# Kernel optimization log

Hardware: AMD Instinct MI355X
Metric: run time of the kernel (lower is better)

The kernel has to match this reference:

```python
import jax, jax.numpy as jnp
import numpy as np

P = 16; N_SIDE = 14; N_PATCH = 196
ENC_DIM = 1024; ENC_DEPTH = 2; ENC_HEADS = 16; ENC_DH = 64
DEC_DIM = 512; DEC_DEPTH = 1; DEC_HEADS = 8; DEC_DH = 64
NUM_MASKED = int(0.75 * N_PATCH)  # 147


def _ln(x, s, b):
    m = jnp.mean(x, axis=-1, keepdims=True)
    v = jnp.var(x, axis=-1, keepdims=True)
    return (x - m) * jax.lax.rsqrt(v + 1e-5) * s + b


def _mha(x, Wqkv, Wo, heads, dh):
    B, N, _ = x.shape
    q, k, v = jnp.split(x @ Wqkv, 3, axis=-1)
    rs = lambda t: t.reshape(B, N, heads, dh).transpose(0, 2, 1, 3)
    q, k, v = rs(q), rs(k), rs(v)
    scores = jnp.einsum('bhqd,bhkd->bhqk', q, k) / jnp.sqrt(jnp.float32(dh))
    att = jax.nn.softmax(scores, axis=-1)
    o = jnp.einsum('bhqk,bhkd->bhqd', att, v).transpose(0, 2, 1, 3).reshape(B, N, heads * dh)
    return o @ Wo


def _transformer(x, params, depth, heads, dh, lnfs, lnfb):
    (ln1s, ln1b, Wqkv, Wo, ln2s, ln2b, W1, b1, W2, b2) = params
    for i in range(depth):
        x = x + _mha(_ln(x, ln1s[i], ln1b[i]), Wqkv[i], Wo[i], heads, dh)
        h = jax.nn.gelu(_ln(x, ln2s[i], ln2b[i]) @ W1[i] + b1[i])
        x = x + h @ W2[i] + b2[i]
    return _ln(x, lnfs, lnfb)


def setup_inputs() -> dict:
    key = jax.random.key(0)
    ks = jax.random.split(key, 24)
    B = 64
    w = lambda k, s: (jax.random.normal(k, s, jnp.float32) * 0.02)
    E, IE = ENC_DIM, ENC_HEADS * ENC_DH
    D, ID = DEC_DIM, DEC_HEADS * DEC_DH
    d = {}
    d['images'] = jax.random.normal(ks[0], (B, 224, 224, 3), jnp.float32)
    d['rand'] = jax.random.uniform(ks[1], (B, N_PATCH), dtype=jnp.float32)
    d['patch_W'] = w(ks[2], (P * P * 3, E)); d['patch_b'] = jnp.zeros((E,), jnp.float32)
    d['pos_emb'] = w(ks[3], (N_PATCH, E))
    d['enc_ln1s'] = jnp.ones((ENC_DEPTH, E), jnp.float32); d['enc_ln1b'] = jnp.zeros((ENC_DEPTH, E), jnp.float32)
    d['enc_Wqkv'] = w(ks[4], (ENC_DEPTH, E, 3 * IE)); d['enc_Wo'] = w(ks[5], (ENC_DEPTH, IE, E))
    d['enc_ln2s'] = jnp.ones((ENC_DEPTH, E), jnp.float32); d['enc_ln2b'] = jnp.zeros((ENC_DEPTH, E), jnp.float32)
    d['enc_W1'] = w(ks[6], (ENC_DEPTH, E, 4 * E)); d['enc_b1'] = jnp.zeros((ENC_DEPTH, 4 * E), jnp.float32)
    d['enc_W2'] = w(ks[7], (ENC_DEPTH, 4 * E, E)); d['enc_b2'] = jnp.zeros((ENC_DEPTH, E), jnp.float32)
    d['enc_lnfs'] = jnp.ones((E,), jnp.float32); d['enc_lnfb'] = jnp.zeros((E,), jnp.float32)
    d['e2d_W'] = w(ks[8], (E, D)); d['e2d_b'] = jnp.zeros((D,), jnp.float32)
    d['mask_token'] = w(ks[9], (D,))
    d['dec_pos'] = w(ks[10], (N_PATCH, D))
    d['dec_ln1s'] = jnp.ones((DEC_DEPTH, D), jnp.float32); d['dec_ln1b'] = jnp.zeros((DEC_DEPTH, D), jnp.float32)
    d['dec_Wqkv'] = w(ks[11], (DEC_DEPTH, D, 3 * ID)); d['dec_Wo'] = w(ks[12], (DEC_DEPTH, ID, D))
    d['dec_ln2s'] = jnp.ones((DEC_DEPTH, D), jnp.float32); d['dec_ln2b'] = jnp.zeros((DEC_DEPTH, D), jnp.float32)
    d['dec_W1'] = w(ks[13], (DEC_DEPTH, D, 4 * D)); d['dec_b1'] = jnp.zeros((DEC_DEPTH, 4 * D), jnp.float32)
    d['dec_W2'] = w(ks[14], (DEC_DEPTH, 4 * D, D)); d['dec_b2'] = jnp.zeros((DEC_DEPTH, D), jnp.float32)
    d['dec_lnfs'] = jnp.ones((D,), jnp.float32); d['dec_lnfb'] = jnp.zeros((D,), jnp.float32)
    d['pix_W'] = w(ks[15], (D, E)); d['pix_b'] = jnp.zeros((E,), jnp.float32)  # pixel_dim == encoder_dim per source
    return d


def reference(images, rand, patch_W, patch_b, pos_emb,
              enc_ln1s, enc_ln1b, enc_Wqkv, enc_Wo, enc_ln2s, enc_ln2b,
              enc_W1, enc_b1, enc_W2, enc_b2, enc_lnfs, enc_lnfb,
              e2d_W, e2d_b, mask_token, dec_pos,
              dec_ln1s, dec_ln1b, dec_Wqkv, dec_Wo, dec_ln2s, dec_ln2b,
              dec_W1, dec_b1, dec_W2, dec_b2, dec_lnfs, dec_lnfb,
              pix_W, pix_b):
    B = images.shape[0]
    # patch embed: [B,224,224,3] -> [B,196,768] -> [B,196,1024]
    x = images.reshape(B, N_SIDE, P, N_SIDE, P, 3).transpose(0, 1, 3, 2, 4, 5).reshape(B, N_PATCH, P * P * 3)
    patches = x @ patch_W + patch_b
    tokens = patches + pos_emb
    # random masking via argsort of uniform noise
    order = jnp.argsort(rand, axis=-1)
    m_idx = order[:, :NUM_MASKED]        # [B,147]
    u_idx = order[:, NUM_MASKED:]        # [B,49]
    unmasked = jnp.take_along_axis(tokens, u_idx[:, :, None], axis=1)
    enc_params = (enc_ln1s, enc_ln1b, enc_Wqkv, enc_Wo, enc_ln2s, enc_ln2b, enc_W1, enc_b1, enc_W2, enc_b2)
    encoded = _transformer(unmasked, enc_params, ENC_DEPTH, ENC_HEADS, ENC_DH, enc_lnfs, enc_lnfb)
    dec_tok = encoded @ e2d_W + e2d_b + dec_pos[u_idx]
    mask_toks = mask_token + dec_pos[m_idx]
    bidx = jnp.arange(B)[:, None]
    all_tok = jnp.zeros((B, N_PATCH, DEC_DIM), dec_tok.dtype)
    all_tok = all_tok.at[bidx, u_idx].set(dec_tok)
    all_tok = all_tok.at[bidx, m_idx].set(mask_toks)
    dec_params = (dec_ln1s, dec_ln1b, dec_Wqkv, dec_Wo, dec_ln2s, dec_ln2b, dec_W1, dec_b1, dec_W2, dec_b2)
    decoded = _transformer(all_tok, dec_params, DEC_DEPTH, DEC_HEADS, DEC_DH, dec_lnfs, dec_lnfb)
    pred = jnp.take_along_axis(decoded, m_idx[:, :, None], axis=1) @ pix_W + pix_b
    target = jnp.take_along_axis(patches, m_idx[:, :, None], axis=1)
    return jnp.mean((pred - target) ** 2)
```

## Files before the change

### kernel.cpp

```cpp
#include <hip/hip_runtime.h>

typedef __attribute__((ext_vector_type(8))) __bf16 bf16x8;
typedef __attribute__((ext_vector_type(4))) float f32x4;

#define OFF_PATCH 0ull
#define OFF_X     25690112ull
#define OFF_LN    51380224ull
#define OFF_QKV   64225280ull
#define OFF_HID   103022592ull
#define OFF_WP    154402816ull
#define OFF_ORD   214695936ull
#define OFF_PART  214746112ull

#define WP_PATCH   0ull
#define WP_ENC_QKV 786432ull
#define WP_ENC_WO  7077888ull
#define WP_ENC_W1  9175040ull
#define WP_ENC_W2  17563648ull
#define WP_E2D     25952256ull
#define WP_DEC_QKV 26476544ull
#define WP_DEC_WO  27262976ull
#define WP_DEC_W1  27525120ull
#define WP_DEC_W2  28573696ull
#define WP_PIX     29622272ull

#define OM_BF16 0
#define OM_F32  1
#define OM_ACC  2
#define OM_GELU 3

__device__ __forceinline__ float b2f(unsigned short u) {
    return __uint_as_float(((unsigned int)u) << 16);
}
__device__ __forceinline__ unsigned short f2b(float f) {
    unsigned int x = __float_as_uint(f);
    x += 0x7fffu + ((x >> 16) & 1u);
    return (unsigned short)(x >> 16);
}
__device__ __forceinline__ float gelu_f(float x) {
    float u2 = 1.5957691216057308f * x * (1.f + 0.044715f * x * x);
    return x / (1.f + __expf(-u2));
}
__device__ __forceinline__ void gload16(const void* g, void* l) {
    __builtin_amdgcn_global_load_lds((const __attribute__((address_space(1))) void*)g,
                                     (__attribute__((address_space(3))) void*)l, 16, 0, 0);
}

struct PackArgs {
    const float* src[15];
    unsigned long long dstOff[15];
    int K[15], N[15];
    int tileStart[16];
};
__global__ __launch_bounds__(256) void pack_all(PackArgs pa, unsigned short* __restrict__ wp) {
    __shared__ float tile[32][33];
    int t = blockIdx.x;
    int d = 0;
    while (d < 14 && t >= pa.tileStart[d + 1]) ++d;
    int local = t - pa.tileStart[d];
    int K = pa.K[d], N = pa.N[d];
    int ntn = N >> 5;
    int kt = (local / ntn) << 5, nt = (local % ntn) << 5;
    const float* in = pa.src[d];
    unsigned short* out = wp + pa.dstOff[d];
    int tx = threadIdx.x & 31, ty = threadIdx.x >> 5;
#pragma unroll
    for (int i = 0; i < 32; i += 8) tile[ty + i][tx] = in[(size_t)(kt + ty + i) * N + nt + tx];
    __syncthreads();
#pragma unroll
    for (int i = 0; i < 32; i += 8)
        out[(size_t)(nt + ty + i) * K + kt + tx] = f2b(tile[tx][ty + i]);
}

__global__ __launch_bounds__(256) void patchify_kernel(const float* __restrict__ img,
                                                       unsigned short* __restrict__ Xp) {
    const long long total = 12544ll * 768;
    for (long long e = (long long)blockIdx.x * 256 + threadIdx.x; e < total;
         e += (long long)gridDim.x * 256) {
        int row = (int)(e / 768), k = (int)(e % 768);
        int b = row / 196, pi = row % 196;
        int py = pi / 14, px = pi % 14;
        int r = k / 48, rem = k % 48;
        int c = rem / 3, ch = rem % 3;
        long long src = (((long long)(b * 224 + py * 16 + r)) * 224 + (px * 16 + c)) * 3 + ch;
        Xp[e] = f2b(img[src]);
    }
}

template <int OM, bool ATOMIC, bool GATHER>
__global__ __launch_bounds__(512) void gemmV(const unsigned short* __restrict__ A,
                                             const unsigned short* __restrict__ Bt,
                                             void* __restrict__ Cv,
                                             const float* __restrict__ bias,
                                             const int* __restrict__ gord,
                                             int M, int N, int K, int Kc) {
    __shared__ __align__(16) unsigned short S[2 * 128 * 64];
    const int tid = threadIdx.x, w = tid >> 6, lane = tid & 63;
    const int wm = w >> 1, wn = w & 1;
    int nwg = gridDim.x * gridDim.y;
    int orig = blockIdx.y * gridDim.x + blockIdx.x;
    int q = nwg >> 3, r8 = nwg & 7, xcd = orig & 7, off = orig >> 3;
    int wg = (xcd < r8 ? xcd * (q + 1) : r8 * (q + 1) + (xcd - r8) * q) + off;
    const int brow = (wg / gridDim.x) * 128, bcol = (wg % gridDim.x) * 128;
    const int kBeg = blockIdx.z * Kc;
    const int fr = lane & 15, fq = lane >> 4;
    const int lr = lane >> 3;
    const int sca = ((lane & 7) ^ lr) * 8;
    const unsigned short* Agp[2];
#pragma unroll
    for (int i = 0; i < 2; ++i) {
        int r = brow + w * 16 + i * 8 + lr;
        if (r > M - 1) r = M - 1;
        if constexpr (GATHER) {
            int bb = r / 147, jj = r - bb * 147;
            r = bb * 196 + gord[bb * 196 + jj];
        }
        Agp[i] = A + (size_t)r * K + kBeg + sca;
    }
    const unsigned short* Bgp[2];
#pragma unroll
    for (int i = 0; i < 2; ++i) {
        int r = bcol + w * 16 + i * 8 + lr;
        Bgp[i] = Bt + (size_t)r * K + kBeg + sca;
    }

    f32x4 acc[2][4];
#pragma unroll
    for (int m = 0; m < 2; ++m)
#pragma unroll
        for (int n = 0; n < 4; ++n) acc[m][n] = (f32x4){0.f, 0.f, 0.f, 0.f};

    const char* lds = (const char*)S;
    const int sw = (fr & 7) << 4;
    const int a0 = (wm * 32 + fr) * 128 + ((fq * 16) ^ sw);
    const int b0 = 16384 + (wn * 64 + fr) * 128 + ((fq * 16) ^ sw);

    const int nt = Kc >> 6;
    for (int t = 0; t < nt; ++t) {
        __syncthreads();
        const int k0 = t << 6;
#pragma unroll
        for (int i = 0; i < 2; ++i)
            gload16(Agp[i] + k0, S + (w * 16 + i * 8) * 64);
#pragma unroll
        for (int i = 0; i < 2; ++i)
            gload16(Bgp[i] + k0, S + 128 * 64 + (w * 16 + i * 8) * 64);
        __syncthreads();
#pragma unroll
        for (int kk = 0; kk < 2; ++kk) {
            const int kx = kk * 64;
            bf16x8 af[2], bf[4];
#pragma unroll
            for (int m = 0; m < 2; ++m)
                af[m] = *(const bf16x8*)(lds + ((a0 ^ kx) + m * 2048));
#pragma unroll
            for (int n = 0; n < 4; ++n)
                bf[n] = *(const bf16x8*)(lds + ((b0 ^ kx) + n * 2048));
#pragma unroll
            for (int m = 0; m < 2; ++m)
#pragma unroll
                for (int n = 0; n < 4; ++n)
                    acc[m][n] = __builtin_amdgcn_mfma_f32_16x16x32_bf16(af[m], bf[n],
                                                                       acc[m][n], 0, 0, 0);
        }
    }

    const bool addBias = (bias != nullptr) && (kBeg == 0);
#pragma unroll
    for (int m = 0; m < 2; ++m) {
        int rb = brow + wm * 32 + m * 16 + fq * 4;
#pragma unroll
        for (int r = 0; r < 4; ++r) {
            int row = rb + r;
            if (row < M) {
#pragma unroll
                for (int n = 0; n < 4; ++n) {
                    int col = bcol + wn * 64 + n * 16 + fr;
                    float v = acc[m][n][r];
                    if (addBias) v += bias[col];
                    size_t o = (size_t)row * N + col;
                    if constexpr (ATOMIC) atomicAdd((float*)Cv + o, v);
                    else if constexpr (OM == OM_BF16) ((unsigned short*)Cv)[o] = f2b(v);
                    else if constexpr (OM == OM_F32) ((float*)Cv)[o] = v;
                    else if constexpr (OM == OM_ACC) ((float*)Cv)[o] += v;
                    else ((unsigned short*)Cv)[o] = f2b(gelu_f(v));
                }
            }
        }
    }
}

template <int OM>
__global__ __launch_bounds__(256) void gemm3s(const unsigned short* __restrict__ A,
                                              const unsigned short* __restrict__ Bt,
                                              void* __restrict__ Cv,
                                              const float* __restrict__ bias,
                                              int M, int N, int K) {
    __shared__ __align__(16) unsigned short S[2 * 128 * 64];
    const int tid = threadIdx.x, wave = tid >> 6, lane = tid & 63;
    int nwg = gridDim.x * gridDim.y;
    int orig = blockIdx.y * gridDim.x + blockIdx.x;
    int q = nwg >> 3, r8 = nwg & 7, xcd = orig & 7, off = orig >> 3;
    int wg = (xcd < r8 ? xcd * (q + 1) : r8 * (q + 1) + (xcd - r8) * q) + off;
    const int brow = (wg / gridDim.x) * 128, bcol = (wg % gridDim.x) * 128;
    const int fr = lane & 15, fq = lane >> 4;
    const int wr = (wave >> 1) * 64, wc = (wave & 1) * 64;
    const int lr = lane >> 3;
    const int sca = ((lane & 7) ^ lr) * 8;
    const unsigned short* Agp[4];
#pragma unroll
    for (int i = 0; i < 4; ++i) {
        int r = brow + wave * 32 + i * 8 + lr;
        if (r > M - 1) r = M - 1;
        Agp[i] = A + (size_t)r * K + sca;
    }
    const unsigned short* Bgp[4];
#pragma unroll
    for (int i = 0; i < 4; ++i) {
        int r = bcol + wave * 32 + i * 8 + lr;
        Bgp[i] = Bt + (size_t)r * K + sca;
    }
    f32x4 acc[4][4];
#pragma unroll
    for (int m = 0; m < 4; ++m)
#pragma unroll
        for (int n = 0; n < 4; ++n) acc[m][n] = (f32x4){0.f, 0.f, 0.f, 0.f};
    const char* lds = (const char*)S;
    const int sw = (fr & 7) << 4;
    const int a0 = (wr + fr) * 128 + ((fq * 16) ^ sw);
    const int b0 = 16384 + (wc + fr) * 128 + ((fq * 16) ^ sw);
    const int nt = K >> 6;
    for (int t = 0; t < nt; ++t) {
        __syncthreads();
        const int k0 = t << 6;
#pragma unroll
        for (int i = 0; i < 4; ++i) {
            gload16(Agp[i] + k0, S + (wave * 32 + i * 8) * 64);
            gload16(Bgp[i] + k0, S + 128 * 64 + (wave * 32 + i * 8) * 64);
        }
        __syncthreads();
#pragma unroll
        for (int kk = 0; kk < 2; ++kk) {
            const int kx = kk * 64;
            bf16x8 af[4], bf[4];
#pragma unroll
            for (int m = 0; m < 4; ++m) af[m] = *(const bf16x8*)(lds + ((a0 ^ kx) + m * 2048));
#pragma unroll
            for (int n = 0; n < 4; ++n) bf[n] = *(const bf16x8*)(lds + ((b0 ^ kx) + n * 2048));
#pragma unroll
            for (int m = 0; m < 4; ++m)
#pragma unroll
                for (int n = 0; n < 4; ++n)
                    acc[m][n] = __builtin_amdgcn_mfma_f32_16x16x32_bf16(af[m], bf[n],
                                                                       acc[m][n], 0, 0, 0);
        }
    }
#pragma unroll
    for (int m = 0; m < 4; ++m) {
        int rb = brow + wr + m * 16 + fq * 4;
#pragma unroll
        for (int r = 0; r < 4; ++r) {
            int row = rb + r;
            if (row < M) {
#pragma unroll
                for (int n = 0; n < 4; ++n) {
                    int col = bcol + wc + n * 16 + fr;
                    float v = acc[m][n][r];
                    if (bias) v += bias[col];
                    size_t o = (size_t)row * N + col;
                    if constexpr (OM == OM_F32) ((float*)Cv)[o] = v;
                    else ((unsigned short*)Cv)[o] = f2b(v);
                }
            }
        }
    }
}

template <int N, int H, int NW>
__global__ __launch_bounds__(NW * 64) void attn_mfma(const unsigned short* __restrict__ qkv,
                                                     unsigned short* __restrict__ out) {
    constexpr int Npad = ((N + 31) / 32) * 32;
    constexpr int NT = Npad / 16;
    constexpr int KS = Npad / 32;
    constexpr int PS = Npad + 8;
    constexpr int SQ = 3 * H * 64, SO = H * 64;
    __shared__ __align__(16) unsigned short Kl[Npad * 64];
    __shared__ __align__(16) unsigned short Vt[64 * PS];
    __shared__ __align__(16) unsigned short Pl[NW * 16 * PS];
    const int b = blockIdx.x / H, h = blockIdx.x % H;
    const unsigned short* base = qkv + (size_t)b * N * SQ;
    const int qoff = h * 64, koff = (H + h) * 64, voff = (2 * H + h) * 64;
    const int tid = threadIdx.x, wave = tid >> 6, lane = tid & 63;
    const int fr = lane & 15, fq = lane >> 4;

    for (int idx = tid; idx < Npad * 8; idx += NW * 64) {
        int row = idx >> 3, ch = idx & 7;
        uint4 v = {0u, 0u, 0u, 0u};
        if (row < N) v = *(const uint4*)(base + (size_t)row * SQ + koff + ch * 8);
        *(uint4*)((char*)Kl + row * 128 + ((ch * 16) ^ ((row & 7) << 4))) = v;
    }
    for (int idx = tid; idx < Npad * 32; idx += NW * 64) {
        int key = idx >> 5, d2 = (idx & 31) * 2;
        unsigned int v = 0;
        if (key < N) v = *(const unsigned int*)(base + (size_t)key * SQ + voff + d2);
        Vt[d2 * PS + key] = (unsigned short)(v & 0xffffu);
        Vt[(d2 + 1) * PS + key] = (unsigned short)(v >> 16);
    }
    __syncthreads();

    unsigned short* pw = Pl + wave * 16 * PS;
    for (int qt = wave; qt < NT; qt += NW) {
        const int q0 = qt * 16;
        int qr = q0 + fr;
        if (qr > N - 1) qr = N - 1;
        const unsigned short* qp = base + (size_t)qr * SQ + qoff + fq * 8;
        bf16x8 aq0 = *(const bf16x8*)qp;
        bf16x8 aq1 = *(const bf16x8*)(qp + 32);
        f32x4 sa[NT];
#pragma unroll
        for (int ct = 0; ct < NT; ++ct) sa[ct] = (f32x4){0.f, 0.f, 0.f, 0.f};
#pragma unroll
        for (int ct = 0; ct < NT; ++ct) {
            const char* kb = (const char*)Kl + (ct * 16 + fr) * 128;
            bf16x8 kf0 = *(const bf16x8*)(kb + ((fq * 16) ^ ((fr & 7) << 4)));
            bf16x8 kf1 = *(const bf16x8*)(kb + ((64 + fq * 16) ^ ((fr & 7) << 4)));
            sa[ct] = __builtin_amdgcn_mfma_f32_16x16x32_bf16(aq0, kf0, sa[ct], 0, 0, 0);
            sa[ct] = __builtin_amdgcn_mfma_f32_16x16x32_bf16(aq1, kf1, sa[ct], 0, 0, 0);
        }
        float mrow[4] = {-3e38f, -3e38f, -3e38f, -3e38f};
#pragma unroll
        for (int ct = 0; ct < NT; ++ct) {
            bool ok = (ct * 16 + fr) < N;
#pragma unroll
            for (int r = 0; r < 4; ++r) {
                float s = ok ? sa[ct][r] * 0.125f : -3e38f;
                sa[ct][r] = s;
                mrow[r] = fmaxf(mrow[r], s);
            }
        }
#pragma unroll
        for (int off = 1; off <= 8; off <<= 1)
#pragma unroll
            for (int r = 0; r < 4; ++r) mrow[r] = fmaxf(mrow[r], __shfl_xor(mrow[r], off));
        float ssum[4] = {0.f, 0.f, 0.f, 0.f};
#pragma unroll
        for (int ct = 0; ct < NT; ++ct)
#pragma unroll
            for (int r = 0; r < 4; ++r) {
                float p = __expf(sa[ct][r] - mrow[r]);
                sa[ct][r] = p;
                ssum[r] += p;
            }
#pragma unroll
        for (int off = 1; off <= 8; off <<= 1)
#pragma unroll
            for (int r = 0; r < 4; ++r) ssum[r] += __shfl_xor(ssum[r], off);
#pragma unroll
        for (int ct = 0; ct < NT; ++ct)
#pragma unroll
            for (int r = 0; r < 4; ++r)
                pw[(fq * 4 + r) * PS + ct * 16 + fr] = f2b(sa[ct][r]);
        f32x4 oa[4];
#pragma unroll
        for (int vt = 0; vt < 4; ++vt) oa[vt] = (f32x4){0.f, 0.f, 0.f, 0.f};
#pragma unroll
        for (int ks = 0; ks < KS; ++ks) {
            bf16x8 pa = *(const bf16x8*)(pw + fr * PS + ks * 32 + fq * 8);
#pragma unroll
            for (int vt = 0; vt < 4; ++vt) {
                bf16x8 vf = *(const bf16x8*)(&Vt[(vt * 16 + fr) * PS + ks * 32 + fq * 8]);
                oa[vt] = __builtin_amdgcn_mfma_f32_16x16x32_bf16(pa, vf, oa[vt], 0, 0, 0);
            }
        }
        float inv[4];
#pragma unroll
        for (int r = 0; r < 4; ++r) inv[r] = 1.f / ssum[r];
#pragma unroll
        for (int vt = 0; vt < 4; ++vt)
#pragma unroll
            for (int r = 0; r < 4; ++r) {
                int q = q0 + fq * 4 + r;
                if (q < N)
                    out[((size_t)b * N + q) * SO + h * 64 + vt * 16 + fr] =
                        f2b(oa[vt][r] * inv[r]);
            }
    }
}

__global__ __launch_bounds__(256) void argsort_kernel(const float* __restrict__ rnd,
                                                      int* __restrict__ ord) {
    __shared__ float vals[196];
    int b = blockIdx.x, t = threadIdx.x;
    if (t < 196) vals[t] = rnd[b * 196 + t];
    __syncthreads();
    if (t < 196) {
        float v = vals[t];
        int rank = 0;
        for (int j = 0; j < 196; ++j) {
            float vj = vals[j];
            rank += (vj < v) || (vj == v && j < t);
        }
        ord[b * 196 + rank] = t;
    }
}

__global__ __launch_bounds__(256) void gather_unmasked(const unsigned short* __restrict__ patches,
                                                       const float* __restrict__ pos,
                                                       const int* __restrict__ ord,
                                                       float* __restrict__ xe) {
    int row = blockIdx.x;
    int b = row / 49, i = row % 49;
    int src = ord[b * 196 + 147 + i];
    const unsigned short* pr = patches + ((size_t)(b * 196 + src) << 10);
    const float* pe = pos + ((size_t)src << 10);
    float* o = xe + ((size_t)row << 10);
    int d = threadIdx.x * 4;
    ushort4 pv = *(const ushort4*)(pr + d);
    float4 p4 = *(const float4*)(pe + d);
    float4 r;
    r.x = b2f(pv.x) + p4.x; r.y = b2f(pv.y) + p4.y;
    r.z = b2f(pv.z) + p4.z; r.w = b2f(pv.w) + p4.w;
    *(float4*)(o + d) = r;
}

template <int L>
__global__ __launch_bounds__(256) void ln_kernel(const float* __restrict__ x,
                                                 unsigned short* __restrict__ y,
                                                 const float* __restrict__ sw,
                                                 const float* __restrict__ bw) {
    __shared__ float red[8];
    const int tid = threadIdx.x;
    const float* xr = x + (size_t)blockIdx.x * L;
    float sum = 0.f, sq = 0.f;
    for (int i = tid * 4; i < L; i += 1024) {
        float4 v = *(const float4*)(xr + i);
        sum += v.x + v.y + v.z + v.w;
        sq += v.x * v.x + v.y * v.y + v.z * v.z + v.w * v.w;
    }
    for (int off = 32; off; off >>= 1) {
        sum += __shfl_xor(sum, off);
        sq += __shfl_xor(sq, off);
    }
    int wave = tid >> 6, lane = tid & 63;
    if (lane == 0) { red[wave] = sum; red[4 + wave] = sq; }
    __syncthreads();
    float ts = red[0] + red[1] + red[2] + red[3];
    float tq = red[4] + red[5] + red[6] + red[7];
    float mean = ts / L;
    float inv = rsqrtf(tq / L - mean * mean + 1e-5f);
    unsigned short* yr = y + (size_t)blockIdx.x * L;
    for (int i = tid * 4; i < L; i += 1024) {
        float4 v = *(const float4*)(xr + i);
        float4 s4 = *(const float4*)(sw + i);
        float4 b4 = *(const float4*)(bw + i);
        ushort4 o;
        o.x = f2b((v.x - mean) * inv * s4.x + b4.x);
        o.y = f2b((v.y - mean) * inv * s4.y + b4.y);
        o.z = f2b((v.z - mean) * inv * s4.z + b4.z);
        o.w = f2b((v.w - mean) * inv * s4.w + b4.w);
        *(ushort4*)(yr + i) = o;
    }
}

__global__ __launch_bounds__(256) void scatter_tokens(const float* __restrict__ dec_tok,
                                                      const float* __restrict__ dec_pos,
                                                      const float* __restrict__ mask_tok,
                                                      const int* __restrict__ ord,
                                                      float* __restrict__ all_tok) {
    int e = blockIdx.x;
    int b = e / 196, i = e % 196;
    int idx = ord[e];
    float* o = all_tok + ((size_t)(b * 196 + idx)) * 512;
    const float* dp = dec_pos + (size_t)idx * 512;
    int d = threadIdx.x * 4;
    if (d < 512) {
        float4 dv = *(const float4*)(dp + d);
        float4 sv;
        if (i < 147) sv = *(const float4*)(mask_tok + d);
        else sv = *(const float4*)(dec_tok + ((size_t)(b * 49 + (i - 147))) * 512 + d);
        float4 r = {sv.x + dv.x, sv.y + dv.y, sv.z + dv.z, sv.w + dv.w};
        *(float4*)(o + d) = r;
    }
}

__global__ __launch_bounds__(256) void loss_partial(const float* __restrict__ pred,
                                                    const unsigned short* __restrict__ patches,
                                                    const int* __restrict__ ord,
                                                    float* __restrict__ part) {
    __shared__ float red[8];
    float local = 0.f;
    const long long total = 9633792ll;
    for (long long e = (long long)blockIdx.x * 256 + threadIdx.x; e < total; e += 4096ll * 256) {
        int r = (int)(e >> 10), d = (int)(e & 1023);
        int b = r / 147, j = r % 147;
        int idx = ord[b * 196 + j];
        float t = b2f(patches[(((size_t)(b * 196 + idx)) << 10) + d]);
        float df = pred[e] - t;
        local += df * df;
    }
    for (int off = 32; off; off >>= 1) local += __shfl_xor(local, off);
    int wave = threadIdx.x >> 6, lane = threadIdx.x & 63;
    if (lane == 0) red[wave] = local;
    __syncthreads();
    if (threadIdx.x == 0) part[blockIdx.x] = red[0] + red[1] + red[2] + red[3];
}

__global__ __launch_bounds__(256) void loss_final(const float* __restrict__ part,
                                                  float* __restrict__ out) {
    __shared__ float red[8];
    float local = 0.f;
    for (int i = threadIdx.x; i < 4096; i += 256) local += part[i];
    for (int off = 32; off; off >>= 1) local += __shfl_xor(local, off);
    int wave = threadIdx.x >> 6, lane = threadIdx.x & 63;
    if (lane == 0) red[wave] = local;
    __syncthreads();
    if (threadIdx.x == 0) out[0] = (red[0] + red[1] + red[2] + red[3]) / 9633792.0f;
}

extern "C" void kernel_launch(void* const* d_in, const int* in_sizes, int n_in, void* d_out,
                              int out_size, void* d_ws, size_t ws_size, hipStream_t stream) {
    const float* images = (const float*)d_in[0];
    const float* rnd = (const float*)d_in[1];
    const float* patch_W = (const float*)d_in[2];
    const float* patch_b = (const float*)d_in[3];
    const float* pos_emb = (const float*)d_in[4];
    const float* enc_ln1s = (const float*)d_in[5];
    const float* enc_ln1b = (const float*)d_in[6];
    const float* enc_Wqkv = (const float*)d_in[7];
    const float* enc_Wo = (const float*)d_in[8];
    const float* enc_ln2s = (const float*)d_in[9];
    const float* enc_ln2b = (const float*)d_in[10];
    const float* enc_W1 = (const float*)d_in[11];
    const float* enc_b1 = (const float*)d_in[12];
    const float* enc_W2 = (const float*)d_in[13];
    const float* enc_b2 = (const float*)d_in[14];
    const float* enc_lnfs = (const float*)d_in[15];
    const float* enc_lnfb = (const float*)d_in[16];
    const float* e2d_W = (const float*)d_in[17];
    const float* e2d_b = (const float*)d_in[18];
    const float* mask_tok = (const float*)d_in[19];
    const float* dec_pos = (const float*)d_in[20];
    const float* dec_ln1s = (const float*)d_in[21];
    const float* dec_ln1b = (const float*)d_in[22];
    const float* dec_Wqkv = (const float*)d_in[23];
    const float* dec_Wo = (const float*)d_in[24];
    const float* dec_ln2s = (const float*)d_in[25];
    const float* dec_ln2b = (const float*)d_in[26];
    const float* dec_W1 = (const float*)d_in[27];
    const float* dec_b1 = (const float*)d_in[28];
    const float* dec_W2 = (const float*)d_in[29];
    const float* dec_b2 = (const float*)d_in[30];
    const float* dec_lnfs = (const float*)d_in[31];
    const float* dec_lnfb = (const float*)d_in[32];
    const float* pix_W = (const float*)d_in[33];
    const float* pix_b = (const float*)d_in[34];

    char* ws = (char*)d_ws;
    unsigned short* patches = (unsigned short*)(ws + OFF_PATCH);
    float* Rx = (float*)(ws + OFF_X);
    unsigned short* Rln = (unsigned short*)(ws + OFF_LN);
    unsigned short* RqkvB = (unsigned short*)(ws + OFF_QKV);
    float* RqkvF = (float*)(ws + OFF_QKV);
    unsigned short* Rhid = (unsigned short*)(ws + OFF_HID);
    unsigned short* wp = (unsigned short*)(ws + OFF_WP);
    int* ord = (int*)(ws + OFF_ORD);
    float* part = (float*)(ws + OFF_PART);
    float* out = (float*)d_out;

    PackArgs pa;
    int nd = 0, tiles = 0;
    auto ADDP = [&](const float* src, unsigned long long wpo, int K, int N) {
        pa.src[nd] = src; pa.dstOff[nd] = wpo; pa.K[nd] = K; pa.N[nd] = N;
        pa.tileStart[nd] = tiles;
        tiles += (K >> 5) * (N >> 5);
        ++nd;
    };
    ADDP(patch_W, WP_PATCH, 768, 1024);
    for (int l = 0; l < 2; ++l) {
        ADDP(enc_Wqkv + (size_t)l * 1024 * 3072, WP_ENC_QKV + (size_t)l * 3145728, 1024, 3072);
        ADDP(enc_Wo + (size_t)l * 1024 * 1024, WP_ENC_WO + (size_t)l * 1048576, 1024, 1024);
        ADDP(enc_W1 + (size_t)l * 1024 * 4096, WP_ENC_W1 + (size_t)l * 4194304, 1024, 4096);
        ADDP(enc_W2 + (size_t)l * 4096 * 1024, WP_ENC_W2 + (size_t)l * 4194304, 4096, 1024);
    }
    ADDP(e2d_W, WP_E2D, 1024, 512);
    ADDP(dec_Wqkv, WP_DEC_QKV, 512, 1536);
    ADDP(dec_Wo, WP_DEC_WO, 512, 512);
    ADDP(dec_W1, WP_DEC_W1, 512, 2048);
    ADDP(dec_W2, WP_DEC_W2, 2048, 512);
    ADDP(pix_W, WP_PIX, 512, 1024);
    pa.tileStart[nd] = tiles;
    pack_all<<<tiles, 256, 0, stream>>>(pa, wp);

    auto GEMM = [&](int om, const unsigned short* A, size_t wpo, void* C, const float* bias,
                    int M, int N, int K, int S, bool small, const int* gord = nullptr) {
        const unsigned short* Bt = wp + wpo;
        int Kc = K / S;
        if (!small) {
            dim3 g(N / 128, (M + 127) / 128, S);
            if (gord) gemmV<OM_F32, false, true><<<g, 512, 0, stream>>>(A, Bt, C, bias, gord, M, N, K, Kc);
            else if (S > 1) gemmV<OM_ACC, true, false><<<g, 512, 0, stream>>>(A, Bt, C, bias, nullptr, M, N, K, Kc);
            else if (om == OM_BF16) gemmV<OM_BF16, false, false><<<g, 512, 0, stream>>>(A, Bt, C, bias, nullptr, M, N, K, Kc);
            else if (om == OM_F32) gemmV<OM_F32, false, false><<<g, 512, 0, stream>>>(A, Bt, C, bias, nullptr, M, N, K, Kc);
            else if (om == OM_ACC) gemmV<OM_ACC, false, false><<<g, 512, 0, stream>>>(A, Bt, C, bias, nullptr, M, N, K, Kc);
            else gemmV<OM_GELU, false, false><<<g, 512, 0, stream>>>(A, Bt, C, bias, nullptr, M, N, K, Kc);
        } else {
            dim3 g(N / 128, (M + 127) / 128, 1);
            if (om == OM_F32) gemm3s<OM_F32><<<g, 256, 0, stream>>>(A, Bt, C, bias, M, N, K);
            else gemm3s<OM_BF16><<<g, 256, 0, stream>>>(A, Bt, C, bias, M, N, K);
        }
    };

    patchify_kernel<<<4096, 256, 0, stream>>>(images, Rhid);
    GEMM(OM_BF16, Rhid, WP_PATCH, patches, patch_b, 12544, 1024, 768, 1, false);
    argsort_kernel<<<64, 256, 0, stream>>>(rnd, ord);
    gather_unmasked<<<3136, 256, 0, stream>>>(patches, pos_emb, ord, Rx);

    for (int l = 0; l < 2; ++l) {
        ln_kernel<1024><<<3136, 256, 0, stream>>>(Rx, Rln, enc_ln1s + l * 1024,
                                                  enc_ln1b + l * 1024);
        GEMM(OM_BF16, Rln, WP_ENC_QKV + (size_t)l * 3145728, RqkvB, nullptr, 3136, 3072, 1024,
             1, false);
        attn_mfma<49, 16, 4><<<64 * 16, 256, 0, stream>>>(RqkvB, Rhid);
        GEMM(OM_ACC, Rhid, WP_ENC_WO + (size_t)l * 1048576, Rx, nullptr, 3136, 1024, 1024, 4,
             false);
        ln_kernel<1024><<<3136, 256, 0, stream>>>(Rx, Rln, enc_ln2s + l * 1024,
                                                  enc_ln2b + l * 1024);
        GEMM(OM_GELU, Rln, WP_ENC_W1 + (size_t)l * 4194304, Rhid, enc_b1 + l * 4096, 3136,
             4096, 1024, 1, false);
        GEMM(OM_ACC, Rhid, WP_ENC_W2 + (size_t)l * 4194304, Rx, enc_b2 + l * 1024, 3136, 1024,
             4096, 4, false);
    }
    ln_kernel<1024><<<3136, 256, 0, stream>>>(Rx, Rln, enc_lnfs, enc_lnfb);

    GEMM(OM_F32, Rln, WP_E2D, RqkvF, e2d_b, 3136, 512, 1024, 1, true);
    scatter_tokens<<<12544, 256, 0, stream>>>(RqkvF, dec_pos, mask_tok, ord, Rx);

    ln_kernel<512><<<12544, 256, 0, stream>>>(Rx, Rln, dec_ln1s, dec_ln1b);
    GEMM(OM_BF16, Rln, WP_DEC_QKV, RqkvB, nullptr, 12544, 1536, 512, 1, false);
    attn_mfma<196, 8, 8><<<64 * 8, 512, 0, stream>>>(RqkvB, Rhid);
    GEMM(OM_ACC, Rhid, WP_DEC_WO, Rx, nullptr, 12544, 512, 512, 2, false);
    ln_kernel<512><<<12544, 256, 0, stream>>>(Rx, Rln, dec_ln2s, dec_ln2b);
    GEMM(OM_GELU, Rln, WP_DEC_W1, Rhid, dec_b1, 12544, 2048, 512, 1, false);
    GEMM(OM_ACC, Rhid, WP_DEC_W2, Rx, dec_b2, 12544, 512, 2048, 2, false);
    ln_kernel<512><<<12544, 256, 0, stream>>>(Rx, Rln, dec_lnfs, dec_lnfb);

    GEMM(OM_F32, Rln, WP_PIX, RqkvF, pix_b, 9408, 1024, 512, 1, false, ord);
    loss_partial<<<4096, 256, 0, stream>>>(RqkvF, patches, ord, part);
    loss_final<<<1, 256, 0, stream>>>(part, out);
}
```

Baseline: 844.9 us.

## Rewrite main GEMM to use 32x32x16 MFMA with 4 waves per block

The main 128x128 tiled GEMM kernel changes from 8 waves, each issuing 16x16x32 MFMAs over a 32x64 subtile, to 4 waves that each compute a 64x64 subtile with four 32x32x16 MFMAs. Each wave now loads twice as many global rows per K-step, and the LDS read pattern and epilogue indexing are adapted to the 32x32 accumulator layout. The aim is fewer LDS fragment reads per FLOP and better MFMA throughput. In exchange there are fewer waves per block for latency hiding and more accumulator registers per thread.

```diff
diff --git a/kernel.cpp b/kernel.cpp
--- a/kernel.cpp
+++ b/kernel.cpp
@@ -2,6 +2,7 @@
 
 typedef __attribute__((ext_vector_type(8))) __bf16 bf16x8;
 typedef __attribute__((ext_vector_type(4))) float f32x4;
+typedef __attribute__((ext_vector_type(16))) float f32x16;
 
 #define OFF_PATCH 0ull
 #define OFF_X     25690112ull
@@ -88,28 +89,28 @@
 }
 
 template <int OM, bool ATOMIC, bool GATHER>
-__global__ __launch_bounds__(512) void gemmV(const unsigned short* __restrict__ A,
+__global__ __launch_bounds__(256) void gemmU(const unsigned short* __restrict__ A,
                                              const unsigned short* __restrict__ Bt,
                                              void* __restrict__ Cv,
                                              const float* __restrict__ bias,
                                              const int* __restrict__ gord,
                                              int M, int N, int K, int Kc) {
     __shared__ __align__(16) unsigned short S[2 * 128 * 64];
-    const int tid = threadIdx.x, w = tid >> 6, lane = tid & 63;
-    const int wm = w >> 1, wn = w & 1;
+    const int tid = threadIdx.x, wave = tid >> 6, lane = tid & 63;
+    const int wm = wave >> 1, wn = wave & 1;
     int nwg = gridDim.x * gridDim.y;
     int orig = blockIdx.y * gridDim.x + blockIdx.x;
     int q = nwg >> 3, r8 = nwg & 7, xcd = orig & 7, off = orig >> 3;
     int wg = (xcd < r8 ? xcd * (q + 1) : r8 * (q + 1) + (xcd - r8) * q) + off;
     const int brow = (wg / gridDim.x) * 128, bcol = (wg % gridDim.x) * 128;
     const int kBeg = blockIdx.z * Kc;
-    const int fr = lane & 15, fq = lane >> 4;
+    const int l31 = lane & 31, hi = lane >> 5;
     const int lr = lane >> 3;
     const int sca = ((lane & 7) ^ lr) * 8;
-    const unsigned short* Agp[2];
-#pragma unroll
-    for (int i = 0; i < 2; ++i) {
-        int r = brow + w * 16 + i * 8 + lr;
+    const unsigned short* Agp[4];
+#pragma unroll
+    for (int i = 0; i < 4; ++i) {
+        int r = brow + wave * 32 + i * 8 + lr;
         if (r > M - 1) r = M - 1;
         if constexpr (GATHER) {
             int bb = r / 147, jj = r - bb * 147;
@@ -117,74 +118,66 @@
         }
         Agp[i] = A + (size_t)r * K + kBeg + sca;
     }
-    const unsigned short* Bgp[2];
-#pragma unroll
-    for (int i = 0; i < 2; ++i) {
-        int r = bcol + w * 16 + i * 8 + lr;
+    const unsigned short* Bgp[4];
+#pragma unroll
+    for (int i = 0; i < 4; ++i) {
+        int r = bcol + wave * 32 + i * 8 + lr;
         Bgp[i] = Bt + (size_t)r * K + kBeg + sca;
     }
 
-    f32x4 acc[2][4];
-#pragma unroll
-    for (int m = 0; m < 2; ++m)
-#pragma unroll
-        for (int n = 0; n < 4; ++n) acc[m][n] = (f32x4){0.f, 0.f, 0.f, 0.f};
+    f32x16 accA, accB, accC, accD;
+#pragma unroll
+    for (int i = 0; i < 16; ++i) { accA[i] = 0.f; accB[i] = 0.f; accC[i] = 0.f; accD[i] = 0.f; }
 
     const char* lds = (const char*)S;
-    const int sw = (fr & 7) << 4;
-    const int a0 = (wm * 32 + fr) * 128 + ((fq * 16) ^ sw);
-    const int b0 = 16384 + (wn * 64 + fr) * 128 + ((fq * 16) ^ sw);
+    const int sw = (l31 & 7) << 4;
+    const int a0 = (wm * 64 + l31) * 128;
+    const int b0 = 16384 + (wn * 64 + l31) * 128;
 
     const int nt = Kc >> 6;
     for (int t = 0; t < nt; ++t) {
         __syncthreads();
         const int k0 = t << 6;
 #pragma unroll
-        for (int i = 0; i < 2; ++i)
-            gload16(Agp[i] + k0, S + (w * 16 + i * 8) * 64);
-#pragma unroll
-        for (int i = 0; i < 2; ++i)
-            gload16(Bgp[i] + k0, S + 128 * 64 + (w * 16 + i * 8) * 64);
+        for (int i = 0; i < 4; ++i)
+            gload16(Agp[i] + k0, S + (wave * 32 + i * 8) * 64);
+#pragma unroll
+        for (int i = 0; i < 4; ++i)
+            gload16(Bgp[i] + k0, S + 128 * 64 + (wave * 32 + i * 8) * 64);
         __syncthreads();
 #pragma unroll
-        for (int kk = 0; kk < 2; ++kk) {
-            const int kx = kk * 64;
-            bf16x8 af[2], bf[4];
-#pragma unroll
-            for (int m = 0; m < 2; ++m)
-                af[m] = *(const bf16x8*)(lds + ((a0 ^ kx) + m * 2048));
-#pragma unroll
-            for (int n = 0; n < 4; ++n)
-                bf[n] = *(const bf16x8*)(lds + ((b0 ^ kx) + n * 2048));
-#pragma unroll
-            for (int m = 0; m < 2; ++m)
-#pragma unroll
-                for (int n = 0; n < 4; ++n)
-                    acc[m][n] = __builtin_amdgcn_mfma_f32_16x16x32_bf16(af[m], bf[n],
-                                                                       acc[m][n], 0, 0, 0);
+        for (int kk = 0; kk < 4; ++kk) {
+            const int ko = (kk * 32 + hi * 16) ^ sw;
+            bf16x8 af0 = *(const bf16x8*)(lds + a0 + ko);
+            bf16x8 af1 = *(const bf16x8*)(lds + a0 + 4096 + ko);
+            bf16x8 bf0 = *(const bf16x8*)(lds + b0 + ko);
+            bf16x8 bf1 = *(const bf16x8*)(lds + b0 + 4096 + ko);
+            accA = __builtin_amdgcn_mfma_f32_32x32x16_bf16(af0, bf0, accA, 0, 0, 0);
+            accB = __builtin_amdgcn_mfma_f32_32x32x16_bf16(af0, bf1, accB, 0, 0, 0);
+            accC = __builtin_amdgcn_mfma_f32_32x32x16_bf16(af1, bf0, accC, 0, 0, 0);
+            accD = __builtin_amdgcn_mfma_f32_32x32x16_bf16(af1, bf1, accD, 0, 0, 0);
         }
     }
 
     const bool addBias = (bias != nullptr) && (kBeg == 0);
-#pragma unroll
-    for (int m = 0; m < 2; ++m) {
-        int rb = brow + wm * 32 + m * 16 + fq * 4;
-#pragma unroll
-        for (int r = 0; r < 4; ++r) {
-            int row = rb + r;
+    const f32x16* accs[4] = {&accA, &accB, &accC, &accD};
+#pragma unroll
+    for (int f = 0; f < 4; ++f) {
+        const int mi = f >> 1, ni = f & 1;
+        const f32x16& ac = *accs[f];
+#pragma unroll
+        for (int r = 0; r < 16; ++r) {
+            int row = brow + wm * 64 + mi * 32 + (r & 3) + 8 * (r >> 2) + 4 * hi;
             if (row < M) {
-#pragma unroll
-                for (int n = 0; n < 4; ++n) {
-                    int col = bcol + wn * 64 + n * 16 + fr;
-                    float v = acc[m][n][r];
-                    if (addBias) v += bias[col];
-                    size_t o = (size_t)row * N + col;
-                    if constexpr (ATOMIC) atomicAdd((float*)Cv + o, v);
-                    else if constexpr (OM == OM_BF16) ((unsigned short*)Cv)[o] = f2b(v);
-                    else if constexpr (OM == OM_F32) ((float*)Cv)[o] = v;
-                    else if constexpr (OM == OM_ACC) ((float*)Cv)[o] += v;
-                    else ((unsigned short*)Cv)[o] = f2b(gelu_f(v));
-                }
+                int col = bcol + wn * 64 + ni * 32 + l31;
+                float v = ac[r];
+                if (addBias) v += bias[col];
+                size_t o = (size_t)row * N + col;
+                if constexpr (ATOMIC) atomicAdd((float*)Cv + o, v);
+                else if constexpr (OM == OM_BF16) ((unsigned short*)Cv)[o] = f2b(v);
+                else if constexpr (OM == OM_F32) ((float*)Cv)[o] = v;
+                else if constexpr (OM == OM_ACC) ((float*)Cv)[o] += v;
+                else ((unsigned short*)Cv)[o] = f2b(gelu_f(v));
             }
         }
     }
@@ -597,12 +590,12 @@
         int Kc = K / S;
         if (!small) {
             dim3 g(N / 128, (M + 127) / 128, S);
-            if (gord) gemmV<OM_F32, false, true><<<g, 512, 0, stream>>>(A, Bt, C, bias, gord, M, N, K, Kc);
-            else if (S > 1) gemmV<OM_ACC, true, false><<<g, 512, 0, stream>>>(A, Bt, C, bias, nullptr, M, N, K, Kc);
-            else if (om == OM_BF16) gemmV<OM_BF16, false, false><<<g, 512, 0, stream>>>(A, Bt, C, bias, nullptr, M, N, K, Kc);
-            else if (om == OM_F32) gemmV<OM_F32, false, false><<<g, 512, 0, stream>>>(A, Bt, C, bias, nullptr, M, N, K, Kc);
-            else if (om == OM_ACC) gemmV<OM_ACC, false, false><<<g, 512, 0, stream>>>(A, Bt, C, bias, nullptr, M, N, K, Kc);
-            else gemmV<OM_GELU, false, false><<<g, 512, 0, stream>>>(A, Bt, C, bias, nullptr, M, N, K, Kc);
+            if (gord) gemmU<OM_F32, false, true><<<g, 256, 0, stream>>>(A, Bt, C, bias, gord, M, N, K, Kc);
+            else if (S > 1) gemmU<OM_ACC, true, false><<<g, 256, 0, stream>>>(A, Bt, C, bias, nullptr, M, N, K, Kc);
+            else if (om == OM_BF16) gemmU<OM_BF16, false, false><<<g, 256, 0, stream>>>(A, Bt, C, bias, nullptr, M, N, K, Kc);
+            else if (om == OM_F32) gemmU<OM_F32, false, false><<<g, 256, 0, stream>>>(A, Bt, C, bias, nullptr, M, N, K, Kc);
+            else if (om == OM_ACC) gemmU<OM_ACC, false, false><<<g, 256, 0, stream>>>(A, Bt, C, bias, nullptr, M, N, K, Kc);
+            else gemmU<OM_GELU, false, false><<<g, 256, 0, stream>>>(A, Bt, C, bias, nullptr, M, N, K, Kc);
         } else {
             dim3 g(N / 128, (M + 127) / 128, 1);
             if (om == OM_F32) gemm3s<OM_F32><<<g, 256, 0, stream>>>(A, Bt, C, bias, M, N, K);
```

New measurement: 972.7 us. +15.1%, slower.

## Fuse MSE loss into pixel-projection GEMM epilogue and use nontemporal stores

Applied to the files above, without the earlier changes.

The pixel-projection GEMM now computes squared error against the gathered target patches directly in its epilogue. It reduces per wave and atomically adds into a single accumulator. This removes the fp32 prediction write/read round trip (~38MB) and the separate partial-reduction kernel. Other GEMM epilogue stores become nontemporal stores, and the loss sum now depends on float atomic ordering.

```diff
diff --git a/kernel.cpp b/kernel.cpp
--- a/kernel.cpp
+++ b/kernel.cpp
@@ -28,6 +28,7 @@
 #define OM_F32  1
 #define OM_ACC  2
 #define OM_GELU 3
+#define OM_LOSS 4
 
 __device__ __forceinline__ float b2f(unsigned short u) {
     return __uint_as_float(((unsigned int)u) << 16);
@@ -93,6 +94,8 @@
                                              void* __restrict__ Cv,
                                              const float* __restrict__ bias,
                                              const int* __restrict__ gord,
+                                             const unsigned short* __restrict__ tgt,
+                                             float* __restrict__ lsum,
                                              int M, int N, int K, int Kc) {
     __shared__ __align__(16) unsigned short S[2 * 128 * 64];
     const int tid = threadIdx.x, w = tid >> 6, lane = tid & 63;
@@ -166,6 +169,7 @@
     }
 
     const bool addBias = (bias != nullptr) && (kBeg == 0);
+    float lloc = 0.f;
 #pragma unroll
     for (int m = 0; m < 2; ++m) {
         int rb = brow + wm * 32 + m * 16 + fq * 4;
@@ -173,20 +177,40 @@
         for (int r = 0; r < 4; ++r) {
             int row = rb + r;
             if (row < M) {
+                size_t prow = 0;
+                if constexpr (OM == OM_LOSS) {
+                    int bb = row / 147, jj = row - bb * 147;
+                    prow = (size_t)(bb * 196 + gord[bb * 196 + jj]);
+                }
 #pragma unroll
                 for (int n = 0; n < 4; ++n) {
                     int col = bcol + wn * 64 + n * 16 + fr;
                     float v = acc[m][n][r];
                     if (addBias) v += bias[col];
-                    size_t o = (size_t)row * N + col;
-                    if constexpr (ATOMIC) atomicAdd((float*)Cv + o, v);
-                    else if constexpr (OM == OM_BF16) ((unsigned short*)Cv)[o] = f2b(v);
-                    else if constexpr (OM == OM_F32) ((float*)Cv)[o] = v;
-                    else if constexpr (OM == OM_ACC) ((float*)Cv)[o] += v;
-                    else ((unsigned short*)Cv)[o] = f2b(gelu_f(v));
+                    if constexpr (OM == OM_LOSS) {
+                        float t = b2f(tgt[(prow << 10) + col]);
+                        float d = v - t;
+                        lloc += d * d;
+                    } else {
+                        size_t o = (size_t)row * N + col;
+                        if constexpr (ATOMIC) atomicAdd((float*)Cv + o, v);
+                        else if constexpr (OM == OM_BF16)
+                            __builtin_nontemporal_store(f2b(v), (unsigned short*)Cv + o);
+                        else if constexpr (OM == OM_F32)
+                            __builtin_nontemporal_store(v, (float*)Cv + o);
+                        else if constexpr (OM == OM_ACC) ((float*)Cv)[o] += v;
+                        else
+                            __builtin_nontemporal_store(f2b(gelu_f(v)),
+                                                        (unsigned short*)Cv + o);
+                    }
                 }
             }
         }
+    }
+    if constexpr (OM == OM_LOSS) {
+#pragma unroll
+        for (int off2 = 32; off2; off2 >>= 1) lloc += __shfl_xor(lloc, off2);
+        if (lane == 0) atomicAdd(lsum, lloc);
     }
 }
 
@@ -483,38 +507,13 @@
     }
 }
 
-__global__ __launch_bounds__(256) void loss_partial(const float* __restrict__ pred,
-                                                    const unsigned short* __restrict__ patches,
-                                                    const int* __restrict__ ord,
-                                                    float* __restrict__ part) {
-    __shared__ float red[8];
-    float local = 0.f;
-    const long long total = 9633792ll;
-    for (long long e = (long long)blockIdx.x * 256 + threadIdx.x; e < total; e += 4096ll * 256) {
-        int r = (int)(e >> 10), d = (int)(e & 1023);
-        int b = r / 147, j = r % 147;
-        int idx = ord[b * 196 + j];
-        float t = b2f(patches[(((size_t)(b * 196 + idx)) << 10) + d]);
-        float df = pred[e] - t;
-        local += df * df;
-    }
-    for (int off = 32; off; off >>= 1) local += __shfl_xor(local, off);
-    int wave = threadIdx.x >> 6, lane = threadIdx.x & 63;
-    if (lane == 0) red[wave] = local;
-    __syncthreads();
-    if (threadIdx.x == 0) part[blockIdx.x] = red[0] + red[1] + red[2] + red[3];
-}
-
-__global__ __launch_bounds__(256) void loss_final(const float* __restrict__ part,
-                                                  float* __restrict__ out) {
-    __shared__ float red[8];
-    float local = 0.f;
-    for (int i = threadIdx.x; i < 4096; i += 256) local += part[i];
-    for (int off = 32; off; off >>= 1) local += __shfl_xor(local, off);
-    int wave = threadIdx.x >> 6, lane = threadIdx.x & 63;
-    if (lane == 0) red[wave] = local;
-    __syncthreads();
-    if (threadIdx.x == 0) out[0] = (red[0] + red[1] + red[2] + red[3]) / 9633792.0f;
+__global__ __launch_bounds__(64) void zero_part(float* __restrict__ part) {
+    part[threadIdx.x] = 0.f;
+}
+
+__global__ __launch_bounds__(64) void loss_final(const float* __restrict__ part,
+                                                 float* __restrict__ out) {
+    if (threadIdx.x == 0) out[0] = part[0] / 9633792.0f;
 }
 
 extern "C" void kernel_launch(void* const* d_in, const int* in_sizes, int n_in, void* d_out,
@@ -592,17 +591,18 @@
     pack_all<<<tiles, 256, 0, stream>>>(pa, wp);
 
     auto GEMM = [&](int om, const unsigned short* A, size_t wpo, void* C, const float* bias,
-                    int M, int N, int K, int S, bool small, const int* gord = nullptr) {
+                    int M, int N, int K, int S, bool small, const int* gord = nullptr,
+                    const unsigned short* tgt = nullptr, float* lsum = nullptr) {
         const unsigned short* Bt = wp + wpo;
         int Kc = K / S;
         if (!small) {
             dim3 g(N / 128, (M + 127) / 128, S);
-            if (gord) gemmV<OM_F32, false, true><<<g, 512, 0, stream>>>(A, Bt, C, bias, gord, M, N, K, Kc);
-            else if (S > 1) gemmV<OM_ACC, true, false><<<g, 512, 0, stream>>>(A, Bt, C, bias, nullptr, M, N, K, Kc);
-            else if (om == OM_BF16) gemmV<OM_BF16, false, false><<<g, 512, 0, stream>>>(A, Bt, C, bias, nullptr, M, N, K, Kc);
-            else if (om == OM_F32) gemmV<OM_F32, false, false><<<g, 512, 0, stream>>>(A, Bt, C, bias, nullptr, M, N, K, Kc);
-            else if (om == OM_ACC) gemmV<OM_ACC, false, false><<<g, 512, 0, stream>>>(A, Bt, C, bias, nullptr, M, N, K, Kc);
-            else gemmV<OM_GELU, false, false><<<g, 512, 0, stream>>>(A, Bt, C, bias, nullptr, M, N, K, Kc);
+            if (om == OM_LOSS) gemmV<OM_LOSS, false, true><<<g, 512, 0, stream>>>(A, Bt, C, bias, gord, tgt, lsum, M, N, K, Kc);
+            else if (S > 1) gemmV<OM_ACC, true, false><<<g, 512, 0, stream>>>(A, Bt, C, bias, nullptr, nullptr, nullptr, M, N, K, Kc);
+            else if (om == OM_BF16) gemmV<OM_BF16, false, false><<<g, 512, 0, stream>>>(A, Bt, C, bias, nullptr, nullptr, nullptr, M, N, K, Kc);
+            else if (om == OM_F32) gemmV<OM_F32, false, false><<<g, 512, 0, stream>>>(A, Bt, C, bias, nullptr, nullptr, nullptr, M, N, K, Kc);
+            else if (om == OM_ACC) gemmV<OM_ACC, false, false><<<g, 512, 0, stream>>>(A, Bt, C, bias, nullptr, nullptr, nullptr, M, N, K, Kc);
+            else gemmV<OM_GELU, false, false><<<g, 512, 0, stream>>>(A, Bt, C, bias, nullptr, nullptr, nullptr, M, N, K, Kc);
         } else {
             dim3 g(N / 128, (M + 127) / 128, 1);
             if (om == OM_F32) gemm3s<OM_F32><<<g, 256, 0, stream>>>(A, Bt, C, bias, M, N, K);
@@ -644,7 +644,7 @@
     GEMM(OM_ACC, Rhid, WP_DEC_W2, Rx, dec_b2, 12544, 512, 2048, 2, false);
     ln_kernel<512><<<12544, 256, 0, stream>>>(Rx, Rln, dec_lnfs, dec_lnfb);
 
-    GEMM(OM_F32, Rln, WP_PIX, RqkvF, pix_b, 9408, 1024, 512, 1, false, ord);
-    loss_partial<<<4096, 256, 0, stream>>>(RqkvF, patches, ord, part);
-    loss_final<<<1, 256, 0, stream>>>(part, out);
-}
+    zero_part<<<1, 64, 0, stream>>>(part);
+    GEMM(OM_LOSS, Rln, WP_PIX, nullptr, pix_b, 9408, 1024, 512, 1, false, ord, patches, part);
+    loss_final<<<1, 64, 0, stream>>>(part, out);
+}
```

New measurement: 939.9 us. 1.11x slower.
